# Kernel tuning notes

Measured on AMD Instinct MI355X. Metric: run time of the kernel, lower is better.

## Reference

```python
import jax, jax.numpy as jnp
import numpy as np

N = 16384   # total queries (= total keys here)
B = 16      # scenes
K = 1024    # keys per scene (key_batch_cnt entries)
L = 32      # local neighborhood size
D = 256     # d_model
H = 8       # nhead
DFF = 1024
LN_EPS = 1e-5


def setup_inputs() -> dict:
    key = jax.random.key(0)
    ks = jax.random.split(key, 32)
    f32 = jnp.float32

    def lin(k, o, i):
        return jax.random.normal(k, (o, i), f32) * 0.02

    idx = jax.random.randint(ks[3], (N, L), 0, K)
    invalid = jax.random.uniform(ks[4], (N, L)) < 0.1
    index_pair = jnp.where(invalid, -1, idx).astype(jnp.int32)

    inp = {
        "tgt": jax.random.normal(ks[0], (N, D), f32),
        "memory": jax.random.normal(ks[1], (N, D), f32),
        "memory_pos_emb": jax.random.normal(ks[2], (N, D), f32),
        "key_batch_cnt": jnp.full((B,), K, dtype=jnp.int32),
        "index_pair": index_pair,
        "index_pair_batch": jnp.repeat(jnp.arange(B, dtype=jnp.int32), K),
        "Wq": lin(ks[5], D, D), "bq": jnp.zeros((D,), f32),
        "Wkc": lin(ks[6], D, D), "bkc": jnp.zeros((D,), f32),
        "Wkp": lin(ks[7], D, D), "bkp": jnp.zeros((D,), f32),
        "Wv": lin(ks[8], D, D), "bv": jnp.zeros((D,), f32),
        "Wo": lin(ks[9], D, D), "bo": jnp.zeros((D,), f32),
        "W1": lin(ks[10], DFF, D), "b1": jnp.zeros((DFF,), f32),
        "W2": lin(ks[11], D, DFF), "b2": jnp.zeros((D,), f32),
        "g2": jnp.ones((D,), f32), "be2": jnp.zeros((D,), f32),
        "g3": jnp.ones((D,), f32), "be3": jnp.zeros((D,), f32),
    }
    return inp


def _ln(x, g, b):
    m = jnp.mean(x, axis=-1, keepdims=True)
    v = jnp.mean((x - m) ** 2, axis=-1, keepdims=True)
    return (x - m) * jax.lax.rsqrt(v + LN_EPS) * g + b


def reference(tgt, memory, memory_pos_emb, key_batch_cnt, index_pair,
              index_pair_batch, Wq, bq, Wkc, bkc, Wkp, bkp, Wv, bv,
              Wo, bo, W1, b1, W2, b2, g2, be2, g3, be3):
    Dh = D // H
    scale = Dh ** -0.5

    # dense projections
    q = tgt @ Wq.T + bq                              # [N, D]
    k = (memory @ Wkc.T + bkc) + (memory_pos_emb @ Wkp.T + bkp)  # content + pos
    v = memory @ Wv.T + bv

    # local-index gather: per-batch indices -> global key indices
    offsets = jnp.concatenate([jnp.zeros((1,), jnp.int32),
                               jnp.cumsum(key_batch_cnt)[:-1].astype(jnp.int32)])
    mask = index_pair < 0                            # [N, L] padded neighbors
    gidx = jnp.where(mask, 0, index_pair + offsets[index_pair_batch][:, None])

    kg = k[gidx].reshape(N, L, H, Dh)                # gathered keys  [N,L,H,Dh]
    vg = v[gidx].reshape(N, L, H, Dh)                # gathered values
    qh = q.reshape(N, H, Dh)

    attn = jnp.einsum('nhd,nlhd->nhl', qh, kg) * scale
    attn = jnp.where(mask[:, None, :], -1e9, attn)
    attn = jax.nn.softmax(attn, axis=-1)
    out = jnp.einsum('nhl,nlhd->nhd', attn, vg).reshape(N, D)
    tgt2 = out @ Wo.T + bo                           # attention out_proj

    x = _ln(tgt + tgt2, g2, be2)
    ff = jax.nn.relu(x @ W1.T + b1) @ W2.T + b2
    return _ln(x + ff, g3, be3)
```

## Files before the change

kernel.cpp:

```cpp
#include <hip/hip_runtime.h>
#include <stdint.h>

#define N_TOT 16384
#define LNEI  32
#define DM    256
#define NH    8
#define DH    32
#define DFF   1024

typedef __attribute__((ext_vector_type(8))) short  short8;
typedef __attribute__((ext_vector_type(4))) float  floatx4;
typedef __attribute__((ext_vector_type(4))) unsigned short ushort4_t;

static __device__ __forceinline__ float b2f(unsigned short u) {
  union { unsigned int u; float f; } x; x.u = ((unsigned int)u) << 16; return x.f;
}
static __device__ __forceinline__ unsigned short f2b(float f) {
  union { float f; unsigned int u; } x; x.f = f;
  unsigned int r = x.u + 0x7fffu + ((x.u >> 16) & 1u);
  return (unsigned short)(r >> 16);
}

#define NSEG 11
struct Seg { const float* src; unsigned short* dst; int cols; int ostride; int ooff; int begin; };
struct SegTable { Seg s[NSEG]; int total; };

__global__ __launch_bounds__(256) void cvt_all(SegTable T) {
  int e = (blockIdx.x * 256 + threadIdx.x) * 4;
  if (e >= T.total) return;
  int si = 0;
  #pragma unroll
  for (int i = 1; i < NSEG; ++i) if (e >= T.s[i].begin) si = i;
  const Seg s = T.s[si];
  const int le = e - s.begin;
  const int row = le / s.cols;
  const int col = le - row * s.cols;
  floatx4 v = *(const floatx4*)(s.src + le);
  ushort4_t o;
  o.x = f2b(v[0]); o.y = f2b(v[1]); o.z = f2b(v[2]); o.w = f2b(v[3]);
  *(ushort4_t*)(s.dst + (size_t)row * s.ostride + s.ooff + col) = o;
}

static __device__ __forceinline__ void gl_lds16(const unsigned short* g, unsigned short* l) {
  __builtin_amdgcn_global_load_lds(
      (const __attribute__((address_space(1))) unsigned int*)g,
      (__attribute__((address_space(3))) unsigned int*)l, 16, 0, 0);
}

template<int BN, bool RELU>
__global__ __launch_bounds__(256) void gemm_tile(
    const unsigned short* __restrict__ A, const unsigned short* __restrict__ W,
    const float* __restrict__ bias, const float* __restrict__ bias2,
    unsigned short* __restrict__ C, int M, int Nd, int K)
{
  constexpr int BM = 128, BK = 32;
  constexpr int MI = (BN == 128) ? 4 : 2;
  constexpr int NI = 4;
  __shared__ unsigned short sA[BM * BK];
  __shared__ unsigned short sB[BN * BK];

  const int w    = threadIdx.x >> 6;
  const int lane = threadIdx.x & 63;
  const int quad = lane >> 4;
  const int l16  = lane & 15;
  const int m0 = blockIdx.x * BM;
  const int n0 = blockIdx.y * BN;
  const int wrow0 = (BN == 128) ? (w >> 1) * 64 : w * 32;
  const int wcol0 = (BN == 128) ? (w & 1) * 64 : 0;

  const int aflat0 = w * 512 + lane * 8;
  const int ar0 = aflat0 >> 5, ac = aflat0 & 31;

  floatx4 acc[MI][NI] = {};

  for (int k0 = 0; k0 < K; k0 += BK) {
    __syncthreads();
    #pragma unroll
    for (int c = 0; c < 2; ++c) {
      const int row = ar0 + c * 64;
      gl_lds16(A + (size_t)(m0 + row) * K + k0 + ac, &sA[(c * 4 + w) * 512]);
    }
    if (BN == 128) {
      #pragma unroll
      for (int c = 0; c < 2; ++c) {
        const int row = ar0 + c * 64;
        gl_lds16(W + (size_t)(n0 + row) * K + k0 + ac, &sB[(c * 4 + w) * 512]);
      }
    } else {
      gl_lds16(W + (size_t)(n0 + ar0) * K + k0 + ac, &sB[w * 512]);
    }
    __syncthreads();

    short8 af[MI], bf[NI];
    #pragma unroll
    for (int mi = 0; mi < MI; ++mi)
      af[mi] = *(const short8*)&sA[(wrow0 + mi * 16 + l16) * BK + quad * 8];
    #pragma unroll
    for (int ni = 0; ni < NI; ++ni)
      bf[ni] = *(const short8*)&sB[(wcol0 + ni * 16 + l16) * BK + quad * 8];
    #pragma unroll
    for (int mi = 0; mi < MI; ++mi)
      #pragma unroll
      for (int ni = 0; ni < NI; ++ni)
        acc[mi][ni] = __builtin_amdgcn_mfma_f32_16x16x32_bf16(af[mi], bf[ni], acc[mi][ni], 0, 0, 0);
  }

  #pragma unroll
  for (int ni = 0; ni < NI; ++ni) {
    const int col = n0 + wcol0 + ni * 16 + l16;
    float bv = bias[col];
    if (bias2) bv += bias2[col];
    #pragma unroll
    for (int mi = 0; mi < MI; ++mi) {
      const int row0 = m0 + wrow0 + mi * 16 + quad * 4;
      #pragma unroll
      for (int i = 0; i < 4; ++i) {
        float v = acc[mi][ni][i] + bv;
        if (RELU) v = fmaxf(v, 0.f);
        C[(size_t)(row0 + i) * Nd + col] = f2b(v);
      }
    }
  }
}

__global__ __launch_bounds__(256) void attn_kernel(
    const unsigned short* __restrict__ q, const unsigned short* __restrict__ k,
    const unsigned short* __restrict__ v,
    const int* __restrict__ key_batch_cnt, const int* __restrict__ index_pair,
    const int* __restrict__ index_pair_batch,
    unsigned short* __restrict__ out)
{
  const int n = blockIdx.x;
  const int t = threadIdx.x;
  __shared__ int   s_gidx[LNEI];
  __shared__ float s_attn[NH][LNEI];
  __shared__ float s_q[DM];

  s_q[t] = b2f(q[(size_t)n * DM + t]);
  if (t < LNEI) {
    const int b = index_pair_batch[n];
    int off = 0;
    for (int i = 0; i < b; ++i) off += key_batch_cnt[i];
    const int ip = index_pair[(size_t)n * LNEI + t];
    s_gidx[t] = (ip < 0) ? -1 : (ip + off);
  }
  __syncthreads();

  const int h = t >> 5;
  const int l = t & 31;
  const int g = s_gidx[l];
  float score;
  if (g < 0) {
    score = -1e9f;
  } else {
    const unsigned short* krow = k + (size_t)g * DM + h * DH;
    float acc = 0.f;
    #pragma unroll
    for (int j = 0; j < DH; ++j) acc += s_q[h * DH + j] * b2f(krow[j]);
    score = acc * 0.17677669529663687f;
  }
  s_attn[h][l] = score;
  __syncthreads();

  float m = -1e30f;
  #pragma unroll
  for (int j = 0; j < LNEI; ++j) m = fmaxf(m, s_attn[h][j]);
  float sum = 0.f;
  #pragma unroll
  for (int j = 0; j < LNEI; ++j) sum += __expf(s_attn[h][j] - m);
  const float a = __expf(score - m) / sum;
  __syncthreads();
  s_attn[h][l] = a;
  __syncthreads();

  const int dh = t & 31;
  float acc = 0.f;
  #pragma unroll
  for (int j = 0; j < LNEI; ++j) {
    int gj = s_gidx[j];
    if (gj < 0) gj = 0;
    acc += s_attn[h][j] * b2f(v[(size_t)gj * DM + h * DH + dh]);
  }
  out[(size_t)n * DM + t] = f2b(acc);
}

template<bool IN1F32, bool OUTF32>
__global__ __launch_bounds__(256) void ln_kernel(
    const void* __restrict__ in1, const unsigned short* __restrict__ in2,
    const float* __restrict__ g, const float* __restrict__ b,
    void* __restrict__ out)
{
  const int n = blockIdx.x;
  const int t = threadIdx.x;
  __shared__ float red[DM];

  float a1;
  if (IN1F32) a1 = ((const float*)in1)[(size_t)n * DM + t];
  else        a1 = b2f(((const unsigned short*)in1)[(size_t)n * DM + t]);
  const float a = a1 + b2f(in2[(size_t)n * DM + t]);
  red[t] = a;
  __syncthreads();
  for (int s = 128; s > 0; s >>= 1) {
    if (t < s) red[t] += red[t + s];
    __syncthreads();
  }
  const float mean = red[0] * (1.0f / DM);
  __syncthreads();
  const float d = a - mean;
  red[t] = d * d;
  __syncthreads();
  for (int s = 128; s > 0; s >>= 1) {
    if (t < s) red[t] += red[t + s];
    __syncthreads();
  }
  const float var = red[0] * (1.0f / DM);
  const float y = d * rsqrtf(var + 1e-5f) * g[t] + b[t];
  if (OUTF32) ((float*)out)[(size_t)n * DM + t] = y;
  else        ((unsigned short*)out)[(size_t)n * DM + t] = f2b(y);
}

extern "C" void kernel_launch(void* const* d_in, const int* in_sizes, int n_in,
                              void* d_out, int out_size, void* d_ws, size_t ws_size,
                              hipStream_t stream) {
  const float* tgt  = (const float*)d_in[0];
  const float* mem  = (const float*)d_in[1];
  const float* pos  = (const float*)d_in[2];
  const int* kbc    = (const int*)d_in[3];
  const int* ipair  = (const int*)d_in[4];
  const int* ipb    = (const int*)d_in[5];
  const float* Wq   = (const float*)d_in[6];
  const float* bq   = (const float*)d_in[7];
  const float* Wkc  = (const float*)d_in[8];
  const float* bkc  = (const float*)d_in[9];
  const float* Wkp  = (const float*)d_in[10];
  const float* bkp  = (const float*)d_in[11];
  const float* Wv   = (const float*)d_in[12];
  const float* bv   = (const float*)d_in[13];
  const float* Wo   = (const float*)d_in[14];
  const float* bo   = (const float*)d_in[15];
  const float* W1   = (const float*)d_in[16];
  const float* b1   = (const float*)d_in[17];
  const float* W2   = (const float*)d_in[18];
  const float* b2   = (const float*)d_in[19];
  const float* g2   = (const float*)d_in[20];
  const float* be2  = (const float*)d_in[21];
  const float* g3   = (const float*)d_in[22];
  const float* be3  = (const float*)d_in[23];

  const size_t NB = (size_t)N_TOT * DM;
  unsigned short* ws = (unsigned short*)d_ws;
  unsigned short* tgt_b = ws;
  unsigned short* ao_b  = ws;
  unsigned short* mem_b = ws + NB;
  unsigned short* t2_b  = ws + NB;
  unsigned short* mp_b  = ws + 2 * NB;
  unsigned short* x_b   = ws + 2 * NB;
  unsigned short* ff_b  = ws + 3 * NB;
  unsigned short* q_b   = ws + 4 * NB;
  unsigned short* k_b   = ws + 5 * NB;
  unsigned short* v_b   = ws + 6 * NB;
  unsigned short* h1_b  = ws + 4 * NB;
  unsigned short* wgt   = ws + 8 * NB;
  unsigned short* Wq_b = wgt;
  unsigned short* Wk_b = wgt + 65536;
  unsigned short* Wv_b = wgt + 65536 + 131072;
  unsigned short* Wo_b = wgt + 2 * 65536 + 131072;
  unsigned short* W1_b = wgt + 3 * 65536 + 131072;
  unsigned short* W2_b = wgt + 3 * 65536 + 131072 + 262144;

  SegTable T;
  int beg = 0, i = 0;
  auto seg = [&](const float* s, unsigned short* d, int cols, int ostride, int ooff, int nelem) {
    T.s[i].src = s; T.s[i].dst = d; T.s[i].cols = cols;
    T.s[i].ostride = ostride; T.s[i].ooff = ooff; T.s[i].begin = beg;
    beg += nelem; ++i;
  };
  seg(tgt, tgt_b, DM, DM, 0,   (int)NB);
  seg(mem, mem_b, DM, DM, 0,   (int)NB);
  seg(mem, mp_b,  DM, 512, 0,  (int)NB);
  seg(pos, mp_b,  DM, 512, DM, (int)NB);
  seg(Wq,  Wq_b,  DM, DM, 0,   65536);
  seg(Wkc, Wk_b,  DM, 512, 0,  65536);
  seg(Wkp, Wk_b,  DM, 512, DM, 65536);
  seg(Wv,  Wv_b,  DM, DM, 0,   65536);
  seg(Wo,  Wo_b,  DM, DM, 0,   65536);
  seg(W1,  W1_b,  DM, DM, 0,   262144);
  seg(W2,  W2_b,  DFF, DFF, 0, 262144);
  T.total = beg;

  dim3 blk(256);
  cvt_all<<<dim3((T.total / 4 + 255) / 256), blk, 0, stream>>>(T);

  dim3 gP(N_TOT / 128, DM / 64);
  dim3 gF(N_TOT / 128, DFF / 128);

  gemm_tile<64, false><<<gP, blk, 0, stream>>>(tgt_b, Wq_b, bq, nullptr, q_b, N_TOT, DM, DM);
  gemm_tile<64, false><<<gP, blk, 0, stream>>>(mp_b, Wk_b, bkc, bkp, k_b, N_TOT, DM, 512);
  gemm_tile<64, false><<<gP, blk, 0, stream>>>(mem_b, Wv_b, bv, nullptr, v_b, N_TOT, DM, DM);
  attn_kernel<<<dim3(N_TOT), blk, 0, stream>>>(q_b, k_b, v_b, kbc, ipair, ipb, ao_b);
  gemm_tile<64, false><<<gP, blk, 0, stream>>>(ao_b, Wo_b, bo, nullptr, t2_b, N_TOT, DM, DM);
  ln_kernel<true, false><<<dim3(N_TOT), blk, 0, stream>>>(tgt, t2_b, g2, be2, x_b);
  gemm_tile<128, true><<<gF, blk, 0, stream>>>(x_b, W1_b, b1, nullptr, h1_b, N_TOT, DFF, DM);
  gemm_tile<64, false><<<gP, blk, 0, stream>>>(h1_b, W2_b, b2, nullptr, ff_b, N_TOT, DM, DFF);
  ln_kernel<false, true><<<dim3(N_TOT), blk, 0, stream>>>(x_b, ff_b, g3, be3, d_out);
}
```

Measured before the change: 302.7 us.

## Vectorize attention, warp-shuffle reductions, BK=64 GEMM loads, reuse memory buffer for V

The attention kernel now reads K and V rows as 16-byte vectors, does the softmax with warp shuffles instead of shared-memory passes, and has each thread write attention-weighted V into a shared buffer that is then summed per column. LayerNorm replaces its tree reductions and many barriers with wave shuffles plus a small partial array. The GEMM loads two K-slices per barrier pair, halving the number of synchronizations. A new lda argument lets the V projection read from the interleaved memory/pos buffer, which removes one conversion segment and the separate memory copy. The attention kernel needs a larger shared buffer (about 33KB), which may reduce occupancy.

Measured after the change: 313.6 us. +3.6%, slower.

```diff
diff --git a/kernel.cpp b/kernel.cpp
--- a/kernel.cpp
+++ b/kernel.cpp
@@ -11,6 +11,7 @@
 typedef __attribute__((ext_vector_type(8))) short  short8;
 typedef __attribute__((ext_vector_type(4))) float  floatx4;
 typedef __attribute__((ext_vector_type(4))) unsigned short ushort4_t;
+typedef __attribute__((ext_vector_type(4))) unsigned int uint4_t;
 
 static __device__ __forceinline__ float b2f(unsigned short u) {
   union { unsigned int u; float f; } x; x.u = ((unsigned int)u) << 16; return x.f;
@@ -20,8 +21,14 @@
   unsigned int r = x.u + 0x7fffu + ((x.u >> 16) & 1u);
   return (unsigned short)(r >> 16);
 }
-
-#define NSEG 11
+static __device__ __forceinline__ float lo16(unsigned int d) {
+  union { unsigned int u; float f; } x; x.u = d << 16; return x.f;
+}
+static __device__ __forceinline__ float hi16(unsigned int d) {
+  union { unsigned int u; float f; } x; x.u = d & 0xffff0000u; return x.f;
+}
+
+#define NSEG 10
 struct Seg { const float* src; unsigned short* dst; int cols; int ostride; int ooff; int begin; };
 struct SegTable { Seg s[NSEG]; int total; };
 
@@ -51,13 +58,13 @@
 __global__ __launch_bounds__(256) void gemm_tile(
     const unsigned short* __restrict__ A, const unsigned short* __restrict__ W,
     const float* __restrict__ bias, const float* __restrict__ bias2,
-    unsigned short* __restrict__ C, int M, int Nd, int K)
+    unsigned short* __restrict__ C, int M, int Nd, int K, int lda)
 {
   constexpr int BM = 128, BK = 32;
   constexpr int MI = (BN == 128) ? 4 : 2;
   constexpr int NI = 4;
-  __shared__ unsigned short sA[BM * BK];
-  __shared__ unsigned short sB[BN * BK];
+  __shared__ unsigned short sA[2][BM * BK];
+  __shared__ unsigned short sB[2][BN * BK];
 
   const int w    = threadIdx.x >> 6;
   const int lane = threadIdx.x & 63;
@@ -73,36 +80,43 @@
 
   floatx4 acc[MI][NI] = {};
 
-  for (int k0 = 0; k0 < K; k0 += BK) {
+  for (int k0 = 0; k0 < K; k0 += 2 * BK) {
     __syncthreads();
     #pragma unroll
-    for (int c = 0; c < 2; ++c) {
-      const int row = ar0 + c * 64;
-      gl_lds16(A + (size_t)(m0 + row) * K + k0 + ac, &sA[(c * 4 + w) * 512]);
-    }
-    if (BN == 128) {
+    for (int half = 0; half < 2; ++half) {
+      const int kk = k0 + half * BK;
       #pragma unroll
       for (int c = 0; c < 2; ++c) {
         const int row = ar0 + c * 64;
-        gl_lds16(W + (size_t)(n0 + row) * K + k0 + ac, &sB[(c * 4 + w) * 512]);
+        gl_lds16(A + (size_t)(m0 + row) * lda + kk + ac, &sA[half][(c * 4 + w) * 512]);
       }
-    } else {
-      gl_lds16(W + (size_t)(n0 + ar0) * K + k0 + ac, &sB[w * 512]);
+      if (BN == 128) {
+        #pragma unroll
+        for (int c = 0; c < 2; ++c) {
+          const int row = ar0 + c * 64;
+          gl_lds16(W + (size_t)(n0 + row) * K + kk + ac, &sB[half][(c * 4 + w) * 512]);
+        }
+      } else {
+        gl_lds16(W + (size_t)(n0 + ar0) * K + kk + ac, &sB[half][w * 512]);
+      }
     }
     __syncthreads();
 
-    short8 af[MI], bf[NI];
-    #pragma unroll
-    for (int mi = 0; mi < MI; ++mi)
-      af[mi] = *(const short8*)&sA[(wrow0 + mi * 16 + l16) * BK + quad * 8];
-    #pragma unroll
-    for (int ni = 0; ni < NI; ++ni)
-      bf[ni] = *(const short8*)&sB[(wcol0 + ni * 16 + l16) * BK + quad * 8];
-    #pragma unroll
-    for (int mi = 0; mi < MI; ++mi)
+    #pragma unroll
+    for (int half = 0; half < 2; ++half) {
+      short8 af[MI], bf[NI];
+      #pragma unroll
+      for (int mi = 0; mi < MI; ++mi)
+        af[mi] = *(const short8*)&sA[half][(wrow0 + mi * 16 + l16) * BK + quad * 8];
       #pragma unroll
       for (int ni = 0; ni < NI; ++ni)
-        acc[mi][ni] = __builtin_amdgcn_mfma_f32_16x16x32_bf16(af[mi], bf[ni], acc[mi][ni], 0, 0, 0);
+        bf[ni] = *(const short8*)&sB[half][(wcol0 + ni * 16 + l16) * BK + quad * 8];
+      #pragma unroll
+      for (int mi = 0; mi < MI; ++mi)
+        #pragma unroll
+        for (int ni = 0; ni < NI; ++ni)
+          acc[mi][ni] = __builtin_amdgcn_mfma_f32_16x16x32_bf16(af[mi], bf[ni], acc[mi][ni], 0, 0, 0);
+    }
   }
 
   #pragma unroll
@@ -132,9 +146,9 @@
 {
   const int n = blockIdx.x;
   const int t = threadIdx.x;
+  __shared__ float s_q[DM];
   __shared__ int   s_gidx[LNEI];
-  __shared__ float s_attn[NH][LNEI];
-  __shared__ float s_q[DM];
+  __shared__ float s_pv[LNEI][DM + 2];
 
   s_q[t] = b2f(q[(size_t)n * DM + t]);
   if (t < LNEI) {
@@ -149,38 +163,53 @@
   const int h = t >> 5;
   const int l = t & 31;
   const int g = s_gidx[l];
-  float score;
-  if (g < 0) {
-    score = -1e9f;
-  } else {
-    const unsigned short* krow = k + (size_t)g * DM + h * DH;
+
+  float qr[DH];
+  #pragma unroll
+  for (int j = 0; j < DH; ++j) qr[j] = s_q[h * DH + j];
+
+  float score = -1e9f;
+  if (g >= 0) {
+    const uint4_t* kp = (const uint4_t*)(k + (size_t)g * DM + h * DH);
     float acc = 0.f;
     #pragma unroll
-    for (int j = 0; j < DH; ++j) acc += s_q[h * DH + j] * b2f(krow[j]);
+    for (int c = 0; c < 4; ++c) {
+      uint4_t d = kp[c];
+      acc += lo16(d.x) * qr[c * 8 + 0] + hi16(d.x) * qr[c * 8 + 1]
+           + lo16(d.y) * qr[c * 8 + 2] + hi16(d.y) * qr[c * 8 + 3]
+           + lo16(d.z) * qr[c * 8 + 4] + hi16(d.z) * qr[c * 8 + 5]
+           + lo16(d.w) * qr[c * 8 + 6] + hi16(d.w) * qr[c * 8 + 7];
+    }
     score = acc * 0.17677669529663687f;
   }
-  s_attn[h][l] = score;
+
+  float mx = score;
+  #pragma unroll
+  for (int msk = 16; msk >= 1; msk >>= 1) mx = fmaxf(mx, __shfl_xor(mx, msk, 64));
+  const float e = __expf(score - mx);
+  float sm = e;
+  #pragma unroll
+  for (int msk = 16; msk >= 1; msk >>= 1) sm += __shfl_xor(sm, msk, 64);
+  const float a = e / sm;
+
+  {
+    const int gv = (g < 0) ? 0 : g;
+    const uint4_t* vp = (const uint4_t*)(v + (size_t)gv * DM + h * DH);
+    float2* dst = (float2*)&s_pv[l][h * DH];
+    #pragma unroll
+    for (int c = 0; c < 4; ++c) {
+      uint4_t d = vp[c];
+      dst[c * 4 + 0] = make_float2(a * lo16(d.x), a * hi16(d.x));
+      dst[c * 4 + 1] = make_float2(a * lo16(d.y), a * hi16(d.y));
+      dst[c * 4 + 2] = make_float2(a * lo16(d.z), a * hi16(d.z));
+      dst[c * 4 + 3] = make_float2(a * lo16(d.w), a * hi16(d.w));
+    }
+  }
   __syncthreads();
 
-  float m = -1e30f;
-  #pragma unroll
-  for (int j = 0; j < LNEI; ++j) m = fmaxf(m, s_attn[h][j]);
-  float sum = 0.f;
-  #pragma unroll
-  for (int j = 0; j < LNEI; ++j) sum += __expf(s_attn[h][j] - m);
-  const float a = __expf(score - m) / sum;
-  __syncthreads();
-  s_attn[h][l] = a;
-  __syncthreads();
-
-  const int dh = t & 31;
   float acc = 0.f;
   #pragma unroll
-  for (int j = 0; j < LNEI; ++j) {
-    int gj = s_gidx[j];
-    if (gj < 0) gj = 0;
-    acc += s_attn[h][j] * b2f(v[(size_t)gj * DM + h * DH + dh]);
-  }
+  for (int j = 0; j < LNEI; ++j) acc += s_pv[j][t];
   out[(size_t)n * DM + t] = f2b(acc);
 }
 
@@ -192,28 +221,27 @@
 {
   const int n = blockIdx.x;
   const int t = threadIdx.x;
-  __shared__ float red[DM];
+  const int wv = t >> 6;
+  __shared__ float part[8];
 
   float a1;
   if (IN1F32) a1 = ((const float*)in1)[(size_t)n * DM + t];
   else        a1 = b2f(((const unsigned short*)in1)[(size_t)n * DM + t]);
   const float a = a1 + b2f(in2[(size_t)n * DM + t]);
-  red[t] = a;
+
+  float s = a;
+  #pragma unroll
+  for (int msk = 32; msk >= 1; msk >>= 1) s += __shfl_xor(s, msk, 64);
+  if ((t & 63) == 0) part[wv] = s;
   __syncthreads();
-  for (int s = 128; s > 0; s >>= 1) {
-    if (t < s) red[t] += red[t + s];
-    __syncthreads();
-  }
-  const float mean = red[0] * (1.0f / DM);
+  const float mean = (part[0] + part[1] + part[2] + part[3]) * (1.0f / DM);
+  const float d = a - mean;
+  float s2 = d * d;
+  #pragma unroll
+  for (int msk = 32; msk >= 1; msk >>= 1) s2 += __shfl_xor(s2, msk, 64);
+  if ((t & 63) == 0) part[4 + wv] = s2;
   __syncthreads();
-  const float d = a - mean;
-  red[t] = d * d;
-  __syncthreads();
-  for (int s = 128; s > 0; s >>= 1) {
-    if (t < s) red[t] += red[t + s];
-    __syncthreads();
-  }
-  const float var = red[0] * (1.0f / DM);
+  const float var = (part[4] + part[5] + part[6] + part[7]) * (1.0f / DM);
   const float y = d * rsqrtf(var + 1e-5f) * g[t] + b[t];
   if (OUTF32) ((float*)out)[(size_t)n * DM + t] = y;
   else        ((unsigned short*)out)[(size_t)n * DM + t] = f2b(y);
@@ -251,7 +279,6 @@
   unsigned short* ws = (unsigned short*)d_ws;
   unsigned short* tgt_b = ws;
   unsigned short* ao_b  = ws;
-  unsigned short* mem_b = ws + NB;
   unsigned short* t2_b  = ws + NB;
   unsigned short* mp_b  = ws + 2 * NB;
   unsigned short* x_b   = ws + 2 * NB;
@@ -276,7 +303,6 @@
     beg += nelem; ++i;
   };
   seg(tgt, tgt_b, DM, DM, 0,   (int)NB);
-  seg(mem, mem_b, DM, DM, 0,   (int)NB);
   seg(mem, mp_b,  DM, 512, 0,  (int)NB);
   seg(pos, mp_b,  DM, 512, DM, (int)NB);
   seg(Wq,  Wq_b,  DM, DM, 0,   65536);
@@ -294,13 +320,13 @@
   dim3 gP(N_TOT / 128, DM / 64);
   dim3 gF(N_TOT / 128, DFF / 128);
 
-  gemm_tile<64, false><<<gP, blk, 0, stream>>>(tgt_b, Wq_b, bq, nullptr, q_b, N_TOT, DM, DM);
-  gemm_tile<64, false><<<gP, blk, 0, stream>>>(mp_b, Wk_b, bkc, bkp, k_b, N_TOT, DM, 512);
-  gemm_tile<64, false><<<gP, blk, 0, stream>>>(mem_b, Wv_b, bv, nullptr, v_b, N_TOT, DM, DM);
+  gemm_tile<64, false><<<gP, blk, 0, stream>>>(tgt_b, Wq_b, bq, nullptr, q_b, N_TOT, DM, DM, DM);
+  gemm_tile<64, false><<<gP, blk, 0, stream>>>(mp_b, Wk_b, bkc, bkp, k_b, N_TOT, DM, 512, 512);
+  gemm_tile<64, false><<<gP, blk, 0, stream>>>(mp_b, Wv_b, bv, nullptr, v_b, N_TOT, DM, DM, 512);
   attn_kernel<<<dim3(N_TOT), blk, 0, stream>>>(q_b, k_b, v_b, kbc, ipair, ipb, ao_b);
-  gemm_tile<64, false><<<gP, blk, 0, stream>>>(ao_b, Wo_b, bo, nullptr, t2_b, N_TOT, DM, DM);
+  gemm_tile<64, false><<<gP, blk, 0, stream>>>(ao_b, Wo_b, bo, nullptr, t2_b, N_TOT, DM, DM, DM);
   ln_kernel<true, false><<<dim3(N_TOT), blk, 0, stream>>>(tgt, t2_b, g2, be2, x_b);
-  gemm_tile<128, true><<<gF, blk, 0, stream>>>(x_b, W1_b, b1, nullptr, h1_b, N_TOT, DFF, DM);
-  gemm_tile<64, false><<<gP, blk, 0, stream>>>(h1_b, W2_b, b2, nullptr, ff_b, N_TOT, DM, DFF);
+  gemm_tile<128, true><<<gF, blk, 0, stream>>>(x_b, W1_b, b1, nullptr, h1_b, N_TOT, DFF, DM, DM);
+  gemm_tile<64, false><<<gP, blk, 0, stream>>>(h1_b, W2_b, b2, nullptr, ff_b, N_TOT, DM, DFF, DFF);
   ln_kernel<false, true><<<dim3(N_TOT), blk, 0, stream>>>(x_b, ff_b, g3, be3, d_out);
 }
```
